# Kernel optimization log

Measured on AMD Instinct MI355X. Metric: run time of the kernel, lower is better.

Reference implementation:

```python
import jax, jax.numpy as jnp
import numpy as np

K = 3  # kernel_size

def setup_inputs() -> dict:
    key = jax.random.key(0)
    k1, k2, k3 = jax.random.split(key, 3)
    B, T, G, F, O = 4, 512, 129, 96, 96
    x = jax.random.normal(k1, (B, T, G, F), dtype=jnp.float32)
    # kaiming_uniform_(a=sqrt(5)) -> bound = sqrt(6/((1+5)*fan_in)) = 1/sqrt(fan_in), fan_in = F*K
    fan_in = F * K
    wb = 1.0 / np.sqrt(fan_in)
    weight = jax.random.uniform(k2, (G, O, F, K), dtype=jnp.float32, minval=-wb, maxval=wb)
    bias = jax.random.uniform(k3, (G, O), dtype=jnp.float32, minval=-wb, maxval=wb)
    return {"x": x, "weight": weight, "bias": bias}

def reference(x, weight, bias):
    # x: [B, T, G, F]; weight: [G, O, F, K]; bias: [G, O]
    B, T, G, F = x.shape
    pad = K // 2
    xp = jnp.pad(x, ((0, 0), (pad, pad), (0, 0), (0, 0)))  # [B, T+2p, G, F]
    # gather K shifted views -> [B, T, G, F, K] (same windows as unfold with padding K//2)
    xw = jnp.stack([xp[:, k:k + T] for k in range(K)], axis=-1)
    out = jnp.einsum('btgfk,gofk->btgo', xw, weight)
    out = out + bias  # broadcast [G, O] over [B, T, G, O]
    return out
```

## Files before the change

kernel.cpp:

```cpp
#include <hip/hip_runtime.h>
#include <hip/hip_bf16.h>

typedef unsigned short ushort_t;
typedef __attribute__((ext_vector_type(8))) short short8;
typedef __attribute__((ext_vector_type(4))) float floatx4;

#define G_  129
#define F_  96
#define O_  96
#define T_  512
#define KD  288
#define LDB 296

__device__ __forceinline__ ushort_t f2bf(float f) {
    unsigned u = __builtin_bit_cast(unsigned, f);
    u += 0x7FFFu + ((u >> 16) & 1u);
    return (ushort_t)(u >> 16);
}

__global__ void wt_permute(const float* __restrict__ w, ushort_t* __restrict__ wt) {
    int i = blockIdx.x * 256 + threadIdx.x;
    const int total = G_ * O_ * KD;
    if (i >= total) return;
    int base = i / KD;
    int kd = i - base * KD;
    int kk = kd / F_;
    int f  = kd - kk * F_;
    wt[i] = f2bf(w[base * KD + f * 3 + kk]);
}

__global__ __launch_bounds__(512, 4) void conv_mfma(
    const float* __restrict__ x, const ushort_t* __restrict__ wt,
    const float* __restrict__ bias, float* __restrict__ out)
{
    __shared__ __align__(16) ushort_t Wl[O_ * LDB];

    const int g    = blockIdx.y;
    const int m0   = blockIdx.x * 256;
    const int tid  = threadIdx.x;
    const int wave = tid >> 6;
    const int lane = tid & 63;
    const int ln   = lane & 15;
    const int q    = lane >> 4;

    {
        const ushort_t* src = wt + (size_t)g * (O_ * KD);
        for (int idx = tid; idx < O_ * 36; idx += 512) {
            int o = idx / 36;
            int s = idx - o * 36;
            *(short8*)&Wl[o * LDB + s * 8] = *(const short8*)&src[o * KD + s * 8];
        }
    }
    __syncthreads();

    const int r0 = m0 + wave * 32 + ln;
    const int r1 = r0 + 16;
    const int b0 = r0 >> 9, t0 = r0 & 511;
    const int b1 = r1 >> 9, t1 = r1 & 511;

    floatx4 acc[2][6];
    #pragma unroll
    for (int s = 0; s < 2; ++s)
        #pragma unroll
        for (int nt = 0; nt < 6; ++nt)
            acc[s][nt] = (floatx4){0.f, 0.f, 0.f, 0.f};

    auto issue = [&](int c, floatx4* f, bool* vld) {
        int kk = c / 3;
        int fb = (c - kk * 3) * 32;
        int tt0 = t0 + kk - 1, tt1 = t1 + kk - 1;
        vld[0] = (unsigned)tt0 < (unsigned)T_;
        vld[1] = (unsigned)tt1 < (unsigned)T_;
        int tc0 = tt0 < 0 ? 0 : (tt0 > T_ - 1 ? T_ - 1 : tt0);
        int tc1 = tt1 < 0 ? 0 : (tt1 > T_ - 1 ? T_ - 1 : tt1);
        const float* p0 = x + ((size_t)((b0 * T_ + tc0) * G_ + g) * F_ + fb + q * 8);
        const float* p1 = x + ((size_t)((b1 * T_ + tc1) * G_ + g) * F_ + fb + q * 8);
        f[0] = *(const floatx4*)p0;
        f[1] = *(const floatx4*)(p0 + 4);
        f[2] = *(const floatx4*)p1;
        f[3] = *(const floatx4*)(p1 + 4);
    };

    floatx4 pf[4];
    bool pv[2];
    issue(0, pf, pv);

    #pragma unroll
    for (int c = 0; c < 9; ++c) {
        floatx4 cur0 = pf[0], cur1 = pf[1], cur2 = pf[2], cur3 = pf[3];
        bool cv0 = pv[0], cv1 = pv[1];
        if (c < 8) issue(c + 1, pf, pv);

        short8 a0, a1;
        a0[0] = (short)f2bf(cur0[0]); a0[1] = (short)f2bf(cur0[1]);
        a0[2] = (short)f2bf(cur0[2]); a0[3] = (short)f2bf(cur0[3]);
        a0[4] = (short)f2bf(cur1[0]); a0[5] = (short)f2bf(cur1[1]);
        a0[6] = (short)f2bf(cur1[2]); a0[7] = (short)f2bf(cur1[3]);
        a1[0] = (short)f2bf(cur2[0]); a1[1] = (short)f2bf(cur2[1]);
        a1[2] = (short)f2bf(cur2[2]); a1[3] = (short)f2bf(cur2[3]);
        a1[4] = (short)f2bf(cur3[0]); a1[5] = (short)f2bf(cur3[1]);
        a1[6] = (short)f2bf(cur3[2]); a1[7] = (short)f2bf(cur3[3]);
        const short8 z = {0, 0, 0, 0, 0, 0, 0, 0};
        if (!cv0) a0 = z;
        if (!cv1) a1 = z;

        #pragma unroll
        for (int nt = 0; nt < 6; ++nt) {
            const short8 bb = *(const short8*)&Wl[(nt * 16 + ln) * LDB + c * 32 + q * 8];
            acc[0][nt] = __builtin_amdgcn_mfma_f32_16x16x32_bf16(a0, bb, acc[0][nt], 0, 0, 0);
            acc[1][nt] = __builtin_amdgcn_mfma_f32_16x16x32_bf16(a1, bb, acc[1][nt], 0, 0, 0);
        }
    }

    #pragma unroll
    for (int s = 0; s < 2; ++s) {
        int mbase = m0 + wave * 32 + s * 16 + q * 4;
        #pragma unroll
        for (int nt = 0; nt < 6; ++nt) {
            int o = nt * 16 + ln;
            float bv = bias[g * O_ + o];
            #pragma unroll
            for (int r = 0; r < 4; ++r) {
                int m = mbase + r;
                out[(size_t)(m * G_ + g) * O_ + o] = acc[s][nt][r] + bv;
            }
        }
    }
}

extern "C" void kernel_launch(void* const* d_in, const int* in_sizes, int n_in,
                              void* d_out, int out_size, void* d_ws, size_t ws_size,
                              hipStream_t stream) {
    const float* x    = (const float*)d_in[0];
    const float* w    = (const float*)d_in[1];
    const float* bias = (const float*)d_in[2];
    float* out = (float*)d_out;
    ushort_t* wt = (ushort_t*)d_ws;

    const int total_w = G_ * O_ * KD;
    wt_permute<<<dim3((total_w + 255) / 256), dim3(256), 0, stream>>>(w, wt);

    dim3 grid(2048 / 256, G_);
    conv_mfma<<<grid, dim3(512), 0, stream>>>(x, wt, bias, out);
}
```

Baseline: 239.2 us.

## Stage bf16 input rows in per-wave LDS slab and reuse across taps

Each wave now loads its 34 time rows (32 outputs plus halo) for one 32-feature chunk once, converts them to bf16 and stores them into a wave-private LDS slab. The three kernel taps then read shifted A fragments from that slab instead of issuing separate global loads and conversions per tap. This aims to cut redundant global/L2 traffic and repeated fp32-to-bf16 conversion by about 3x. The cost is about 23 KB more LDS per block, which may affect occupancy, plus extra LDS write/read traffic. Global loads for the next feature chunk are prefetched while the current one is written.

```diff
diff --git a/kernel.cpp b/kernel.cpp
--- a/kernel.cpp
+++ b/kernel.cpp
@@ -5,17 +5,22 @@
 typedef __attribute__((ext_vector_type(8))) short short8;
 typedef __attribute__((ext_vector_type(4))) float floatx4;
 
-#define G_  129
-#define F_  96
-#define O_  96
-#define T_  512
-#define KD  288
-#define LDB 296
+#define G_   129
+#define F_   96
+#define O_   96
+#define T_   512
+#define KD   288
+#define LDB  296
+#define SROW 40
+#define SLAB (36 * SROW)
 
-__device__ __forceinline__ ushort_t f2bf(float f) {
+__device__ __forceinline__ unsigned f2bf(float f) {
     unsigned u = __builtin_bit_cast(unsigned, f);
     u += 0x7FFFu + ((u >> 16) & 1u);
-    return (ushort_t)(u >> 16);
+    return u >> 16;
+}
+__device__ __forceinline__ unsigned pk2(float a, float b) {
+    return f2bf(a) | (f2bf(b) << 16);
 }
 
 __global__ void wt_permute(const float* __restrict__ w, ushort_t* __restrict__ wt) {
@@ -26,7 +31,7 @@
     int kd = i - base * KD;
     int kk = kd / F_;
     int f  = kd - kk * F_;
-    wt[i] = f2bf(w[base * KD + f * 3 + kk]);
+    wt[i] = (ushort_t)f2bf(w[base * KD + f * 3 + kk]);
 }
 
 __global__ __launch_bounds__(512, 4) void conv_mfma(
@@ -34,6 +39,7 @@
     const float* __restrict__ bias, float* __restrict__ out)
 {
     __shared__ __align__(16) ushort_t Wl[O_ * LDB];
+    __shared__ __align__(16) ushort_t Xs[8 * SLAB];
 
     const int g    = blockIdx.y;
     const int m0   = blockIdx.x * 256;
@@ -53,10 +59,43 @@
     }
     __syncthreads();
 
-    const int r0 = m0 + wave * 32 + ln;
-    const int r1 = r0 + 16;
-    const int b0 = r0 >> 9, t0 = r0 & 511;
-    const int b1 = r1 >> 9, t1 = r1 & 511;
+    const int m0r = m0 + wave * 32;
+    const int b   = m0r >> 9;
+    const int tb  = m0r & 511;
+
+    const float* tp[5];
+    int  laddr[5];
+    bool wr[5], vld[5];
+    #pragma unroll
+    for (int i = 0; i < 5; ++i) {
+        int task = i * 64 + lane;
+        int row = task >> 3;
+        int seg = task & 7;
+        int tl = tb + row - 1;
+        wr[i]  = row < 34;
+        vld[i] = wr[i] && ((unsigned)tl < (unsigned)T_);
+        int tc = tl < 0 ? 0 : (tl > T_ - 1 ? T_ - 1 : tl);
+        tp[i] = x + ((size_t)((b * T_ + tc) * G_ + g) * F_ + seg * 4);
+        laddr[i] = wave * SLAB + row * SROW + seg * 4;
+    }
+
+    auto issueX = [&](int fb, floatx4* v) {
+        #pragma unroll
+        for (int i = 0; i < 5; ++i)
+            v[i] = *(const floatx4*)(tp[i] + fb * 32);
+    };
+    auto writeX = [&](const floatx4* v) {
+        #pragma unroll
+        for (int i = 0; i < 5; ++i) {
+            if (wr[i]) {
+                unsigned lo = pk2(v[i][0], v[i][1]);
+                unsigned hi = pk2(v[i][2], v[i][3]);
+                if (!vld[i]) { lo = 0u; hi = 0u; }
+                uint2 d; d.x = lo; d.y = hi;
+                *(uint2*)&Xs[laddr[i]] = d;
+            }
+        }
+    };
 
     floatx4 acc[2][6];
     #pragma unroll
@@ -65,51 +104,28 @@
         for (int nt = 0; nt < 6; ++nt)
             acc[s][nt] = (floatx4){0.f, 0.f, 0.f, 0.f};
 
-    auto issue = [&](int c, floatx4* f, bool* vld) {
-        int kk = c / 3;
-        int fb = (c - kk * 3) * 32;
-        int tt0 = t0 + kk - 1, tt1 = t1 + kk - 1;
-        vld[0] = (unsigned)tt0 < (unsigned)T_;
-        vld[1] = (unsigned)tt1 < (unsigned)T_;
-        int tc0 = tt0 < 0 ? 0 : (tt0 > T_ - 1 ? T_ - 1 : tt0);
-        int tc1 = tt1 < 0 ? 0 : (tt1 > T_ - 1 ? T_ - 1 : tt1);
-        const float* p0 = x + ((size_t)((b0 * T_ + tc0) * G_ + g) * F_ + fb + q * 8);
-        const float* p1 = x + ((size_t)((b1 * T_ + tc1) * G_ + g) * F_ + fb + q * 8);
-        f[0] = *(const floatx4*)p0;
-        f[1] = *(const floatx4*)(p0 + 4);
-        f[2] = *(const floatx4*)p1;
-        f[3] = *(const floatx4*)(p1 + 4);
-    };
-
-    floatx4 pf[4];
-    bool pv[2];
-    issue(0, pf, pv);
+    floatx4 cur[5], nxt[5];
+    issueX(0, cur);
 
     #pragma unroll
-    for (int c = 0; c < 9; ++c) {
-        floatx4 cur0 = pf[0], cur1 = pf[1], cur2 = pf[2], cur3 = pf[3];
-        bool cv0 = pv[0], cv1 = pv[1];
-        if (c < 8) issue(c + 1, pf, pv);
-
-        short8 a0, a1;
-        a0[0] = (short)f2bf(cur0[0]); a0[1] = (short)f2bf(cur0[1]);
-        a0[2] = (short)f2bf(cur0[2]); a0[3] = (short)f2bf(cur0[3]);
-        a0[4] = (short)f2bf(cur1[0]); a0[5] = (short)f2bf(cur1[1]);
-        a0[6] = (short)f2bf(cur1[2]); a0[7] = (short)f2bf(cur1[3]);
-        a1[0] = (short)f2bf(cur2[0]); a1[1] = (short)f2bf(cur2[1]);
-        a1[2] = (short)f2bf(cur2[2]); a1[3] = (short)f2bf(cur2[3]);
-        a1[4] = (short)f2bf(cur3[0]); a1[5] = (short)f2bf(cur3[1]);
-        a1[6] = (short)f2bf(cur3[2]); a1[7] = (short)f2bf(cur3[3]);
-        const short8 z = {0, 0, 0, 0, 0, 0, 0, 0};
-        if (!cv0) a0 = z;
-        if (!cv1) a1 = z;
+    for (int fb = 0; fb < 3; ++fb) {
+        if (fb < 2) issueX(fb + 1, nxt);
+        writeX(cur);
 
         #pragma unroll
-        for (int nt = 0; nt < 6; ++nt) {
-            const short8 bb = *(const short8*)&Wl[(nt * 16 + ln) * LDB + c * 32 + q * 8];
-            acc[0][nt] = __builtin_amdgcn_mfma_f32_16x16x32_bf16(a0, bb, acc[0][nt], 0, 0, 0);
-            acc[1][nt] = __builtin_amdgcn_mfma_f32_16x16x32_bf16(a1, bb, acc[1][nt], 0, 0, 0);
+        for (int kk = 0; kk < 3; ++kk) {
+            const short8 a0 = *(const short8*)&Xs[wave * SLAB + (ln + kk) * SROW + q * 8];
+            const short8 a1 = *(const short8*)&Xs[wave * SLAB + (16 + ln + kk) * SROW + q * 8];
+            const int c32 = (kk * 3 + fb) * 32;
+            #pragma unroll
+            for (int nt = 0; nt < 6; ++nt) {
+                const short8 bb = *(const short8*)&Wl[(nt * 16 + ln) * LDB + c32 + q * 8];
+                acc[0][nt] = __builtin_amdgcn_mfma_f32_16x16x32_bf16(a0, bb, acc[0][nt], 0, 0, 0);
+                acc[1][nt] = __builtin_amdgcn_mfma_f32_16x16x32_bf16(a1, bb, acc[1][nt], 0, 0, 0);
+            }
         }
+        #pragma unroll
+        for (int i = 0; i < 5; ++i) cur[i] = nxt[i];
     }
 
     #pragma unroll
```

Measured after the change: 218.5 us. 8.6% less time.
